# Kernel tuning notes

Hardware: AMD Instinct MI355X
Metric: run time of the kernel (lower is better)

The kernel has to match this reference:

```python
import jax, jax.numpy as jnp
import numpy as np

FEAT = 512   # PLIP backbone dim
HID = 256
N_CLS_HEADS = 11   # each 3 classes -> 33 logits
N_REG_HEADS = 55   # each 1 output

def _xavier(key, shape):
    fan_in, fan_out = shape[0], shape[1]
    limit = float(np.sqrt(6.0 / (fan_in + fan_out)))
    return jax.random.uniform(key, shape, jnp.float32, -limit, limit)

def setup_inputs() -> dict:
    key = jax.random.key(0)
    ks = jax.random.split(key, 8)
    N = 200000
    x = jax.random.normal(ks[0], (1, N, FEAT), jnp.float32)
    return {
        'x': x,
        'W1': _xavier(ks[1], (FEAT, HID)), 'b1': jnp.zeros((HID,), jnp.float32),
        'Wa': _xavier(ks[2], (HID, HID)), 'ba': jnp.zeros((HID,), jnp.float32),
        'Wb': _xavier(ks[3], (HID, HID)), 'bb': jnp.zeros((HID,), jnp.float32),
        'Wc': _xavier(ks[4], (HID, 1)),  'bc': jnp.zeros((1,), jnp.float32),
        'Wr': _xavier(ks[5], (HID, HID)), 'br': jnp.zeros((HID,), jnp.float32),
        # 11 classifier heads (3 classes each) stacked into one [256, 33] GEMM
        'Wcls': _xavier(ks[6], (HID, 3 * N_CLS_HEADS)), 'bcls': jnp.zeros((3 * N_CLS_HEADS,), jnp.float32),
        'Wreg': _xavier(ks[7], (HID, N_REG_HEADS)), 'breg': jnp.zeros((N_REG_HEADS,), jnp.float32),
    }

def reference(x, W1, b1, Wa, ba, Wb, bb, Wc, bc, Wr, br, Wcls, bcls, Wreg, breg):
    xp = x[0]                                   # [N, 512]
    h = jax.nn.relu(xp @ W1 + b1)               # [N, 256]  (dropout inactive at eval)
    a = jnp.tanh(h @ Wa + ba)                   # [N, 256]
    b = jax.nn.sigmoid(h @ Wb + bb)             # [N, 256]
    A_raw = ((a * b) @ Wc + bc).T               # [1, N]
    A = jax.nn.softmax(A_raw, axis=1)           # [1, N]
    global_feat = A @ h                         # [1, 256]
    hr = jax.nn.relu(global_feat @ Wr + br)     # [1, 256]
    cls_logits = hr @ Wcls + bcls               # [1, 33] = 11 heads x 3 classes
    reg_values = (hr @ Wreg + breg)[0]          # [55]   (per-head squeeze(1))
    return A, global_feat, cls_logits, reg_values
```

## Files before the change

kernel.cpp:

```cpp
#include <hip/hip_runtime.h>
#include <stdint.h>

#define FEAT 512
#define HID  256
#define TILE 64
#define G1   768

typedef __attribute__((ext_vector_type(8))) short   short8;
typedef __attribute__((ext_vector_type(4))) float   floatx4;

__device__ inline unsigned short f2bf(float x){
  union { float f; uint32_t u; } v; v.f = x;
  uint32_t u = v.u;
  u += 0x7FFFu + ((u >> 16) & 1u);
  return (unsigned short)(u >> 16);
}
__device__ inline float bf2f(unsigned short h){
  union { uint32_t u; float f; } v; v.u = ((uint32_t)h) << 16;
  return v.f;
}
__device__ inline float sigm_f(float x){ return 1.f/(1.f + __expf(-x)); }
__device__ inline float tanh_f(float x){ return 2.f/(1.f + __expf(-2.f*x)) - 1.f; }

__global__ void prep_weights(const float* __restrict__ W1, const float* __restrict__ Wa,
                             const float* __restrict__ Wb,
                             unsigned short* __restrict__ W1bf,
                             unsigned short* __restrict__ Wabf,
                             unsigned short* __restrict__ Wbbf){
  int t = blockIdx.x*256 + threadIdx.x;
  const float* src; unsigned short* dst; int g;
  if      (t < 16384){ src = W1; dst = W1bf; g = t; }
  else if (t < 24576){ src = Wa; dst = Wabf; g = t - 16384; }
  else if (t < 32768){ src = Wb; dst = Wbbf; g = t - 24576; }
  else return;
  int lane = g & 63, nt = (g >> 6) & 15, kb = g >> 10;
  int col  = nt*16 + (lane & 15);
  int row0 = kb*32 + (lane >> 4)*8;
  unsigned short* d = dst + (size_t)g*8;
  const float*    s = src + (size_t)row0*HID + col;
  #pragma unroll
  for (int j = 0; j < 8; ++j) d[j] = f2bf(s[(size_t)j*HID]);
}

__global__ __launch_bounds__(256, 3) void fused_main(
    const float* __restrict__ x,
    const float* __restrict__ b1, const float* __restrict__ ba,
    const float* __restrict__ bb, const float* __restrict__ Wc,
    const float* __restrict__ bc,
    const unsigned short* __restrict__ W1bf,
    const unsigned short* __restrict__ Wabf,
    const unsigned short* __restrict__ Wbbf,
    float* __restrict__ s_buf, float* __restrict__ partials, int ntiles)
{
  __shared__ alignas(16) unsigned short Hs[64][264];
  __shared__ alignas(16) unsigned short Ws[8192];
  __shared__ float pbuf[4][16];

  const int tid  = threadIdx.x;
  const int wave = tid >> 6, lane = tid & 63;
  const int quad = lane >> 4, l15 = lane & 15;

  float m_run = -INFINITY, l_run = 0.f;
  float g0 = 0.f, g1 = 0.f, g2 = 0.f, g3 = 0.f;
  const float bcv = bc[0];

  for (int t = blockIdx.x; t < ntiles; t += gridDim.x){
    const int tokw = t*TILE + wave*16;

    floatx4 acc[16];
    #pragma unroll
    for (int nt = 0; nt < 16; ++nt){
      float bv = b1[nt*16 + l15];
      floatx4 tmp = {bv, bv, bv, bv};
      acc[nt] = tmp;
    }
    const float* xrow = x + (size_t)(tokw + l15)*FEAT + quad*8;
    #pragma unroll 1
    for (int kb = 0; kb < 16; ++kb){
      __syncthreads();
      { const short8* srcv = (const short8*)(W1bf + (size_t)kb*8192);
        short8* dstv = (short8*)Ws;
        #pragma unroll
        for (int c = 0; c < 4; ++c) dstv[tid + 256*c] = srcv[tid + 256*c]; }
      __syncthreads();
      const float* xp = xrow + kb*32;
      float4 xa = *(const float4*)xp;
      float4 xb = *(const float4*)(xp + 4);
      union { short8 v; unsigned short u[8]; } af;
      af.u[0]=f2bf(xa.x); af.u[1]=f2bf(xa.y); af.u[2]=f2bf(xa.z); af.u[3]=f2bf(xa.w);
      af.u[4]=f2bf(xb.x); af.u[5]=f2bf(xb.y); af.u[6]=f2bf(xb.z); af.u[7]=f2bf(xb.w);
      #pragma unroll
      for (int nt = 0; nt < 16; ++nt){
        short8 bfv = *(const short8*)&Ws[nt*512 + lane*8];
        acc[nt] = __builtin_amdgcn_mfma_f32_16x16x32_bf16(af.v, bfv, acc[nt], 0, 0, 0);
      }
    }
    #pragma unroll
    for (int nt = 0; nt < 16; ++nt){
      #pragma unroll
      for (int r = 0; r < 4; ++r){
        float hv = fmaxf(acc[nt][r], 0.f);
        Hs[wave*16 + quad*4 + r][nt*16 + l15] = f2bf(hv);
      }
    }

    float sp0 = 0.f, sp1 = 0.f, sp2 = 0.f, sp3 = 0.f;
    #pragma unroll 1
    for (int nh = 0; nh < 2; ++nh){
      floatx4 aacc[8], bacc[8];
      #pragma unroll
      for (int nt = 0; nt < 8; ++nt){
        int col = (nh*8 + nt)*16 + l15;
        float av = ba[col], bv = bb[col];
        floatx4 ta = {av, av, av, av}; aacc[nt] = ta;
        floatx4 tb = {bv, bv, bv, bv}; bacc[nt] = tb;
      }
      #pragma unroll 1
      for (int kb = 0; kb < 8; ++kb){
        __syncthreads();
        { const short8* sA = (const short8*)(Wabf + (size_t)(kb*16 + nh*8)*512);
          const short8* sB = (const short8*)(Wbbf + (size_t)(kb*16 + nh*8)*512);
          short8* dstv = (short8*)Ws;
          dstv[tid]       = sA[tid];
          dstv[tid + 256] = sA[tid + 256];
          dstv[tid + 512] = sB[tid];
          dstv[tid + 768] = sB[tid + 256]; }
        __syncthreads();
        short8 af = *(const short8*)&Hs[wave*16 + l15][kb*32 + quad*8];
        #pragma unroll
        for (int nt = 0; nt < 8; ++nt){
          short8 bA = *(const short8*)&Ws[nt*512 + lane*8];
          short8 bB = *(const short8*)&Ws[4096 + nt*512 + lane*8];
          aacc[nt] = __builtin_amdgcn_mfma_f32_16x16x32_bf16(af, bA, aacc[nt], 0, 0, 0);
          bacc[nt] = __builtin_amdgcn_mfma_f32_16x16x32_bf16(af, bB, bacc[nt], 0, 0, 0);
        }
      }
      #pragma unroll
      for (int nt = 0; nt < 8; ++nt){
        int col = (nh*8 + nt)*16 + l15;
        float wcv = Wc[col];
        sp0 += tanh_f(aacc[nt][0]) * sigm_f(bacc[nt][0]) * wcv;
        sp1 += tanh_f(aacc[nt][1]) * sigm_f(bacc[nt][1]) * wcv;
        sp2 += tanh_f(aacc[nt][2]) * sigm_f(bacc[nt][2]) * wcv;
        sp3 += tanh_f(aacc[nt][3]) * sigm_f(bacc[nt][3]) * wcv;
      }
    }
    #pragma unroll
    for (int mk = 1; mk < 16; mk <<= 1){
      sp0 += __shfl_xor(sp0, mk, 64);
      sp1 += __shfl_xor(sp1, mk, 64);
      sp2 += __shfl_xor(sp2, mk, 64);
      sp3 += __shfl_xor(sp3, mk, 64);
    }
    float s0 = sp0 + bcv, s1 = sp1 + bcv, s2 = sp2 + bcv, s3 = sp3 + bcv;
    if (l15 == 0){
      float* sb = s_buf + tokw + quad*4;
      sb[0] = s0; sb[1] = s1; sb[2] = s2; sb[3] = s3;
    }
    float tmax = fmaxf(fmaxf(s0, s1), fmaxf(s2, s3));
    tmax = fmaxf(tmax, __shfl_xor(tmax, 16, 64));
    tmax = fmaxf(tmax, __shfl_xor(tmax, 32, 64));
    float m_new = fmaxf(m_run, tmax);
    float alpha = __expf(m_run - m_new);
    float p0 = __expf(s0 - m_new), p1 = __expf(s1 - m_new);
    float p2 = __expf(s2 - m_new), p3 = __expf(s3 - m_new);
    float psum = p0 + p1 + p2 + p3;
    psum += __shfl_xor(psum, 16, 64);
    psum += __shfl_xor(psum, 32, 64);
    l_run = l_run*alpha + psum;
    m_run = m_new;
    if (l15 == 0){
      pbuf[wave][quad*4+0] = p0; pbuf[wave][quad*4+1] = p1;
      pbuf[wave][quad*4+2] = p2; pbuf[wave][quad*4+3] = p3;
    }
    g0 *= alpha; g1 *= alpha; g2 *= alpha; g3 *= alpha;
    #pragma unroll
    for (int rw = 0; rw < 16; ++rw){
      float pr = pbuf[wave][rw];
      const unsigned short* hp = &Hs[wave*16 + rw][lane*4];
      g0 += pr*bf2f(hp[0]); g1 += pr*bf2f(hp[1]);
      g2 += pr*bf2f(hp[2]); g3 += pr*bf2f(hp[3]);
    }
  }

  __syncthreads();
  float* fred = (float*)Ws;
  if (lane == 0) fred[wave] = m_run;
  __syncthreads();
  float M = fmaxf(fmaxf(fred[0], fred[1]), fmaxf(fred[2], fred[3]));
  float sc = (m_run == -INFINITY) ? 0.f : __expf(m_run - M);
  if (lane == 0) fred[4 + wave] = l_run * sc;
  fred[8 + wave*256 + lane*4 + 0] = g0*sc;
  fred[8 + wave*256 + lane*4 + 1] = g1*sc;
  fred[8 + wave*256 + lane*4 + 2] = g2*sc;
  fred[8 + wave*256 + lane*4 + 3] = g3*sc;
  __syncthreads();
  float gsum = fred[8 + 0*256 + tid] + fred[8 + 1*256 + tid]
             + fred[8 + 2*256 + tid] + fred[8 + 3*256 + tid];
  float* P = partials + (size_t)blockIdx.x*258;
  if (tid == 0){ P[0] = M; P[1] = fred[4] + fred[5] + fred[6] + fred[7]; }
  P[2 + tid] = gsum;
}

__global__ void reduce_heads(const float* __restrict__ partials,
    const float* __restrict__ Wr,   const float* __restrict__ br,
    const float* __restrict__ Wcls, const float* __restrict__ bcls,
    const float* __restrict__ Wreg, const float* __restrict__ breg,
    float* __restrict__ out, float* __restrict__ ML, int ntok)
{
  __shared__ float red[256];
  __shared__ float scw[G1];
  __shared__ float gf[256];
  __shared__ float hr[256];
  int t = threadIdx.x;

  float lm = -INFINITY;
  for (int i = t; i < G1; i += 256) lm = fmaxf(lm, partials[(size_t)i*258]);
  red[t] = lm; __syncthreads();
  for (int s = 128; s > 0; s >>= 1){ if (t < s) red[t] = fmaxf(red[t], red[t+s]); __syncthreads(); }
  float M = red[0];
  __syncthreads();

  float ll = 0.f;
  for (int i = t; i < G1; i += 256){
    float w = __expf(partials[(size_t)i*258] - M);
    scw[i] = w;
    ll += partials[(size_t)i*258 + 1] * w;
  }
  red[t] = ll; __syncthreads();
  for (int s = 128; s > 0; s >>= 1){ if (t < s) red[t] += red[t+s]; __syncthreads(); }
  float L = red[0];

  float g = 0.f;
  for (int i = 0; i < G1; ++i) g += partials[(size_t)i*258 + 2 + t] * scw[i];
  float gfv = g / L;
  gf[t] = gfv;
  out[ntok + t] = gfv;
  if (t == 0){ ML[0] = M; ML[1] = 1.f / L; }
  __syncthreads();

  float h = br[t];
  for (int c = 0; c < 256; ++c) h += gf[c] * Wr[c*256 + t];
  h = fmaxf(h, 0.f);
  hr[t] = h; __syncthreads();

  if (t < 33){
    float v = bcls[t];
    for (int j = 0; j < 256; ++j) v += hr[j] * Wcls[j*33 + t];
    out[ntok + 256 + t] = v;
  }
  if (t < 55){
    float v = breg[t];
    for (int j = 0; j < 256; ++j) v += hr[j] * Wreg[j*55 + t];
    out[ntok + 289 + t] = v;
  }
}

__global__ void finalize_A(const float* __restrict__ s_buf, const float* __restrict__ ML,
                           float* __restrict__ out, int ntok){
  int i = blockIdx.x*256 + threadIdx.x;
  if (i < ntok) out[i] = __expf(s_buf[i] - ML[0]) * ML[1];
}

extern "C" void kernel_launch(void* const* d_in, const int* in_sizes, int n_in,
                              void* d_out, int out_size, void* d_ws, size_t ws_size,
                              hipStream_t stream){
  (void)n_in; (void)out_size; (void)ws_size;
  const float* x    = (const float*)d_in[0];
  const float* W1   = (const float*)d_in[1];
  const float* b1   = (const float*)d_in[2];
  const float* Wa   = (const float*)d_in[3];
  const float* ba   = (const float*)d_in[4];
  const float* Wb   = (const float*)d_in[5];
  const float* bb   = (const float*)d_in[6];
  const float* Wc   = (const float*)d_in[7];
  const float* bc   = (const float*)d_in[8];
  const float* Wr   = (const float*)d_in[9];
  const float* br   = (const float*)d_in[10];
  const float* Wcls = (const float*)d_in[11];
  const float* bcls = (const float*)d_in[12];
  const float* Wreg = (const float*)d_in[13];
  const float* breg = (const float*)d_in[14];
  float* out = (float*)d_out;

  const int ntok   = in_sizes[0] / FEAT;
  const int ntiles = ntok / TILE;

  char* ws = (char*)d_ws;
  float* s_buf = (float*)ws;
  size_t off = (size_t)ntok * 4;
  float* partials = (float*)(ws + off); off += (size_t)G1*258*4;
  float* ML = (float*)(ws + off); off += 16;
  unsigned short* W1bf = (unsigned short*)(ws + off); off += (size_t)FEAT*HID*2;
  unsigned short* Wabf = (unsigned short*)(ws + off); off += (size_t)HID*HID*2;
  unsigned short* Wbbf = (unsigned short*)(ws + off); off += (size_t)HID*HID*2;

  prep_weights<<<128, 256, 0, stream>>>(W1, Wa, Wb, W1bf, Wabf, Wbbf);
  fused_main<<<G1, 256, 0, stream>>>(x, b1, ba, bb, Wc, bc, W1bf, Wabf, Wbbf,
                                     s_buf, partials, ntiles);
  reduce_heads<<<1, 256, 0, stream>>>(partials, Wr, br, Wcls, bcls, Wreg, breg,
                                      out, ML, ntok);
  finalize_A<<<(ntok + 255)/256, 256, 0, stream>>>(s_buf, ML, out, ntok);
}
```

Baseline: 749.8 us.

## Drop LDS weight staging, process 32-token strips per wave with register-prefetched x

The main kernel no longer stages weight blocks into shared memory behind block-wide barriers. Each wave now reads the bf16 weight fragments straight from global/L2 and handles two 16-token strips at once, so each weight fragment feeds two MFMAs. x loads are double-buffered in registers, and a single-strip path handles the tail. The grid shrinks to 512 blocks with launch bounds of 2 per SIMD, and the reduce kernel is widened to 1024 threads with split reductions. This removes barrier stalls and LDS traffic, at the cost of many more global weight loads and higher register pressure, which lowers occupancy.

After: 866.9 us. 15.6% more time.

```diff
diff --git a/kernel.cpp b/kernel.cpp
--- a/kernel.cpp
+++ b/kernel.cpp
@@ -3,8 +3,7 @@
 
 #define FEAT 512
 #define HID  256
-#define TILE 64
-#define G1   768
+#define G1   512
 
 typedef __attribute__((ext_vector_type(8))) short   short8;
 typedef __attribute__((ext_vector_type(4))) float   floatx4;
@@ -21,6 +20,13 @@
 }
 __device__ inline float sigm_f(float x){ return 1.f/(1.f + __expf(-x)); }
 __device__ inline float tanh_f(float x){ return 2.f/(1.f + __expf(-2.f*x)) - 1.f; }
+
+__device__ inline short8 pack_bf8(float4 a, float4 b){
+  union { short8 v; unsigned short u[8]; } r;
+  r.u[0]=f2bf(a.x); r.u[1]=f2bf(a.y); r.u[2]=f2bf(a.z); r.u[3]=f2bf(a.w);
+  r.u[4]=f2bf(b.x); r.u[5]=f2bf(b.y); r.u[6]=f2bf(b.z); r.u[7]=f2bf(b.w);
+  return r.v;
+}
 
 __global__ void prep_weights(const float* __restrict__ W1, const float* __restrict__ Wa,
                              const float* __restrict__ Wb,
@@ -42,7 +48,207 @@
   for (int j = 0; j < 8; ++j) d[j] = f2bf(s[(size_t)j*HID]);
 }
 
-__global__ __launch_bounds__(256, 3) void fused_main(
+template<bool TWO>
+__device__ __forceinline__ void do_tile(
+    const float* __restrict__ x, int tok0,
+    const unsigned short* __restrict__ W1bf,
+    const unsigned short* __restrict__ Wabf,
+    const unsigned short* __restrict__ Wbbf,
+    const float* __restrict__ b1, const float* __restrict__ ba,
+    const float* __restrict__ bb, const float* __restrict__ Wc, float bcv,
+    float* __restrict__ s_buf,
+    unsigned short (*__restrict__ hs)[264], float* __restrict__ pbufw,
+    int lane, int quad, int l15,
+    float& m_run, float& l_run, float& g0, float& g1, float& g2, float& g3)
+{
+  const short8* w1v = (const short8*)W1bf;
+  const short8* wav = (const short8*)Wabf;
+  const short8* wbv = (const short8*)Wbbf;
+
+  floatx4 acc0[16], acc1[16];
+  #pragma unroll
+  for (int nt = 0; nt < 16; ++nt){
+    float bv = b1[nt*16 + l15];
+    floatx4 t = {bv, bv, bv, bv};
+    acc0[nt] = t;
+    if (TWO) acc1[nt] = t;
+  }
+  const float* xr0 = x + (size_t)(tok0 + l15)*FEAT + quad*8;
+  const float* xr1 = x + (size_t)(tok0 + 16 + l15)*FEAT + quad*8;
+
+  float4 xA0[2], xB0[2], xA1[2], xB1[2];
+  xA0[0] = *(const float4*)(xr0);       xA0[1] = *(const float4*)(xr0 + 4);
+  xB0[0] = *(const float4*)(xr0 + 32);  xB0[1] = *(const float4*)(xr0 + 36);
+  if (TWO){
+    xA1[0] = *(const float4*)(xr1);       xA1[1] = *(const float4*)(xr1 + 4);
+    xB1[0] = *(const float4*)(xr1 + 32);  xB1[1] = *(const float4*)(xr1 + 36);
+  }
+  #pragma unroll 1
+  for (int i = 0; i < 8; ++i){
+    const int kbe = 2*i, kbo = 2*i + 1;
+    short8 af0 = pack_bf8(xA0[0], xA0[1]);
+    short8 af1;
+    if (TWO) af1 = pack_bf8(xA1[0], xA1[1]);
+    if (i < 7){
+      xA0[0] = *(const float4*)(xr0 + (kbe+2)*32);
+      xA0[1] = *(const float4*)(xr0 + (kbe+2)*32 + 4);
+      if (TWO){
+        xA1[0] = *(const float4*)(xr1 + (kbe+2)*32);
+        xA1[1] = *(const float4*)(xr1 + (kbe+2)*32 + 4);
+      }
+    }
+    {
+      const short8* wp = w1v + (size_t)kbe*1024 + lane;
+      #pragma unroll
+      for (int nt = 0; nt < 16; ++nt){
+        short8 wf = wp[nt*64];
+        acc0[nt] = __builtin_amdgcn_mfma_f32_16x16x32_bf16(af0, wf, acc0[nt], 0, 0, 0);
+        if (TWO)
+          acc1[nt] = __builtin_amdgcn_mfma_f32_16x16x32_bf16(af1, wf, acc1[nt], 0, 0, 0);
+      }
+    }
+    short8 bf0 = pack_bf8(xB0[0], xB0[1]);
+    short8 bf1;
+    if (TWO) bf1 = pack_bf8(xB1[0], xB1[1]);
+    if (i < 7){
+      xB0[0] = *(const float4*)(xr0 + (kbo+2)*32);
+      xB0[1] = *(const float4*)(xr0 + (kbo+2)*32 + 4);
+      if (TWO){
+        xB1[0] = *(const float4*)(xr1 + (kbo+2)*32);
+        xB1[1] = *(const float4*)(xr1 + (kbo+2)*32 + 4);
+      }
+    }
+    {
+      const short8* wp = w1v + (size_t)kbo*1024 + lane;
+      #pragma unroll
+      for (int nt = 0; nt < 16; ++nt){
+        short8 wf = wp[nt*64];
+        acc0[nt] = __builtin_amdgcn_mfma_f32_16x16x32_bf16(bf0, wf, acc0[nt], 0, 0, 0);
+        if (TWO)
+          acc1[nt] = __builtin_amdgcn_mfma_f32_16x16x32_bf16(bf1, wf, acc1[nt], 0, 0, 0);
+      }
+    }
+  }
+  #pragma unroll
+  for (int nt = 0; nt < 16; ++nt){
+    #pragma unroll
+    for (int r = 0; r < 4; ++r){
+      hs[quad*4 + r][nt*16 + l15] = f2bf(fmaxf(acc0[nt][r], 0.f));
+      if (TWO) hs[16 + quad*4 + r][nt*16 + l15] = f2bf(fmaxf(acc1[nt][r], 0.f));
+    }
+  }
+
+  float s00=0.f,s01=0.f,s02=0.f,s03=0.f, s10=0.f,s11=0.f,s12=0.f,s13=0.f;
+  #pragma unroll 1
+  for (int nh = 0; nh < 2; ++nh){
+    floatx4 aa0[8], ab0[8], aa1[8], ab1[8];
+    #pragma unroll
+    for (int nt = 0; nt < 8; ++nt){
+      int col = (nh*8 + nt)*16 + l15;
+      float av = ba[col], bv = bb[col];
+      floatx4 ta = {av, av, av, av};
+      floatx4 tb = {bv, bv, bv, bv};
+      aa0[nt] = ta; ab0[nt] = tb;
+      if (TWO){ aa1[nt] = ta; ab1[nt] = tb; }
+    }
+    short8 hf0 = *(const short8*)&hs[l15][quad*8];
+    short8 hf1;
+    if (TWO) hf1 = *(const short8*)&hs[16 + l15][quad*8];
+    #pragma unroll 1
+    for (int kb = 0; kb < 8; ++kb){
+      short8 cf0 = hf0, cf1;
+      if (TWO) cf1 = hf1;
+      if (kb < 7){
+        hf0 = *(const short8*)&hs[l15][(kb+1)*32 + quad*8];
+        if (TWO) hf1 = *(const short8*)&hs[16 + l15][(kb+1)*32 + quad*8];
+      }
+      const short8* wpa = wav + (size_t)(kb*16 + nh*8)*64 + lane;
+      const short8* wpb = wbv + (size_t)(kb*16 + nh*8)*64 + lane;
+      #pragma unroll
+      for (int nt = 0; nt < 8; ++nt){
+        short8 wfa = wpa[nt*64];
+        short8 wfb = wpb[nt*64];
+        aa0[nt] = __builtin_amdgcn_mfma_f32_16x16x32_bf16(cf0, wfa, aa0[nt], 0, 0, 0);
+        ab0[nt] = __builtin_amdgcn_mfma_f32_16x16x32_bf16(cf0, wfb, ab0[nt], 0, 0, 0);
+        if (TWO){
+          aa1[nt] = __builtin_amdgcn_mfma_f32_16x16x32_bf16(cf1, wfa, aa1[nt], 0, 0, 0);
+          ab1[nt] = __builtin_amdgcn_mfma_f32_16x16x32_bf16(cf1, wfb, ab1[nt], 0, 0, 0);
+        }
+      }
+    }
+    #pragma unroll
+    for (int nt = 0; nt < 8; ++nt){
+      float wcv = Wc[(nh*8 + nt)*16 + l15];
+      s00 += tanh_f(aa0[nt][0]) * sigm_f(ab0[nt][0]) * wcv;
+      s01 += tanh_f(aa0[nt][1]) * sigm_f(ab0[nt][1]) * wcv;
+      s02 += tanh_f(aa0[nt][2]) * sigm_f(ab0[nt][2]) * wcv;
+      s03 += tanh_f(aa0[nt][3]) * sigm_f(ab0[nt][3]) * wcv;
+      if (TWO){
+        s10 += tanh_f(aa1[nt][0]) * sigm_f(ab1[nt][0]) * wcv;
+        s11 += tanh_f(aa1[nt][1]) * sigm_f(ab1[nt][1]) * wcv;
+        s12 += tanh_f(aa1[nt][2]) * sigm_f(ab1[nt][2]) * wcv;
+        s13 += tanh_f(aa1[nt][3]) * sigm_f(ab1[nt][3]) * wcv;
+      }
+    }
+  }
+  #pragma unroll
+  for (int mk = 1; mk < 16; mk <<= 1){
+    s00 += __shfl_xor(s00, mk, 64); s01 += __shfl_xor(s01, mk, 64);
+    s02 += __shfl_xor(s02, mk, 64); s03 += __shfl_xor(s03, mk, 64);
+    if (TWO){
+      s10 += __shfl_xor(s10, mk, 64); s11 += __shfl_xor(s11, mk, 64);
+      s12 += __shfl_xor(s12, mk, 64); s13 += __shfl_xor(s13, mk, 64);
+    }
+  }
+  s00 += bcv; s01 += bcv; s02 += bcv; s03 += bcv;
+  if (TWO){ s10 += bcv; s11 += bcv; s12 += bcv; s13 += bcv; }
+  if (l15 == 0){
+    float* sb = s_buf + tok0 + quad*4;
+    sb[0] = s00; sb[1] = s01; sb[2] = s02; sb[3] = s03;
+    if (TWO){
+      float* sb1 = s_buf + tok0 + 16 + quad*4;
+      sb1[0] = s10; sb1[1] = s11; sb1[2] = s12; sb1[3] = s13;
+    }
+  }
+  float tmax = fmaxf(fmaxf(s00, s01), fmaxf(s02, s03));
+  if (TWO) tmax = fmaxf(tmax, fmaxf(fmaxf(s10, s11), fmaxf(s12, s13)));
+  tmax = fmaxf(tmax, __shfl_xor(tmax, 16, 64));
+  tmax = fmaxf(tmax, __shfl_xor(tmax, 32, 64));
+  float m_new = fmaxf(m_run, tmax);
+  float alpha = __expf(m_run - m_new);
+  float p00 = __expf(s00 - m_new), p01 = __expf(s01 - m_new);
+  float p02 = __expf(s02 - m_new), p03 = __expf(s03 - m_new);
+  float psum = p00 + p01 + p02 + p03;
+  float p10, p11, p12, p13;
+  if (TWO){
+    p10 = __expf(s10 - m_new); p11 = __expf(s11 - m_new);
+    p12 = __expf(s12 - m_new); p13 = __expf(s13 - m_new);
+    psum += p10 + p11 + p12 + p13;
+  }
+  psum += __shfl_xor(psum, 16, 64);
+  psum += __shfl_xor(psum, 32, 64);
+  l_run = l_run*alpha + psum;
+  m_run = m_new;
+  if (l15 == 0){
+    pbufw[quad*4+0] = p00; pbufw[quad*4+1] = p01;
+    pbufw[quad*4+2] = p02; pbufw[quad*4+3] = p03;
+    if (TWO){
+      pbufw[16+quad*4+0] = p10; pbufw[16+quad*4+1] = p11;
+      pbufw[16+quad*4+2] = p12; pbufw[16+quad*4+3] = p13;
+    }
+  }
+  g0 *= alpha; g1 *= alpha; g2 *= alpha; g3 *= alpha;
+  constexpr int NR = TWO ? 32 : 16;
+  #pragma unroll
+  for (int rw = 0; rw < NR; ++rw){
+    float pr = pbufw[rw];
+    const unsigned short* hp = &hs[rw][lane*4];
+    g0 += pr*bf2f(hp[0]); g1 += pr*bf2f(hp[1]);
+    g2 += pr*bf2f(hp[2]); g3 += pr*bf2f(hp[3]);
+  }
+}
+
+__global__ __launch_bounds__(256, 2) void fused_main(
     const float* __restrict__ x,
     const float* __restrict__ b1, const float* __restrict__ ba,
     const float* __restrict__ bb, const float* __restrict__ Wc,
@@ -50,141 +256,41 @@
     const unsigned short* __restrict__ W1bf,
     const unsigned short* __restrict__ Wabf,
     const unsigned short* __restrict__ Wbbf,
-    float* __restrict__ s_buf, float* __restrict__ partials, int ntiles)
+    float* __restrict__ s_buf, float* __restrict__ partials, int ntok)
 {
-  __shared__ alignas(16) unsigned short Hs[64][264];
-  __shared__ alignas(16) unsigned short Ws[8192];
-  __shared__ float pbuf[4][16];
+  __shared__ alignas(16) unsigned short Hs[4][32][264];
+  __shared__ float pbuf[4][32];
 
   const int tid  = threadIdx.x;
   const int wave = tid >> 6, lane = tid & 63;
   const int quad = lane >> 4, l15 = lane & 15;
+  const int wid  = blockIdx.x*4 + wave;
+  const int nw   = gridDim.x << 2;
 
   float m_run = -INFINITY, l_run = 0.f;
   float g0 = 0.f, g1 = 0.f, g2 = 0.f, g3 = 0.f;
   const float bcv = bc[0];
 
-  for (int t = blockIdx.x; t < ntiles; t += gridDim.x){
-    const int tokw = t*TILE + wave*16;
-
-    floatx4 acc[16];
-    #pragma unroll
-    for (int nt = 0; nt < 16; ++nt){
-      float bv = b1[nt*16 + l15];
-      floatx4 tmp = {bv, bv, bv, bv};
-      acc[nt] = tmp;
-    }
-    const float* xrow = x + (size_t)(tokw + l15)*FEAT + quad*8;
-    #pragma unroll 1
-    for (int kb = 0; kb < 16; ++kb){
-      __syncthreads();
-      { const short8* srcv = (const short8*)(W1bf + (size_t)kb*8192);
-        short8* dstv = (short8*)Ws;
-        #pragma unroll
-        for (int c = 0; c < 4; ++c) dstv[tid + 256*c] = srcv[tid + 256*c]; }
-      __syncthreads();
-      const float* xp = xrow + kb*32;
-      float4 xa = *(const float4*)xp;
-      float4 xb = *(const float4*)(xp + 4);
-      union { short8 v; unsigned short u[8]; } af;
-      af.u[0]=f2bf(xa.x); af.u[1]=f2bf(xa.y); af.u[2]=f2bf(xa.z); af.u[3]=f2bf(xa.w);
-      af.u[4]=f2bf(xb.x); af.u[5]=f2bf(xb.y); af.u[6]=f2bf(xb.z); af.u[7]=f2bf(xb.w);
-      #pragma unroll
-      for (int nt = 0; nt < 16; ++nt){
-        short8 bfv = *(const short8*)&Ws[nt*512 + lane*8];
-        acc[nt] = __builtin_amdgcn_mfma_f32_16x16x32_bf16(af.v, bfv, acc[nt], 0, 0, 0);
-      }
-    }
-    #pragma unroll
-    for (int nt = 0; nt < 16; ++nt){
-      #pragma unroll
-      for (int r = 0; r < 4; ++r){
-        float hv = fmaxf(acc[nt][r], 0.f);
-        Hs[wave*16 + quad*4 + r][nt*16 + l15] = f2bf(hv);
-      }
-    }
-
-    float sp0 = 0.f, sp1 = 0.f, sp2 = 0.f, sp3 = 0.f;
-    #pragma unroll 1
-    for (int nh = 0; nh < 2; ++nh){
-      floatx4 aacc[8], bacc[8];
-      #pragma unroll
-      for (int nt = 0; nt < 8; ++nt){
-        int col = (nh*8 + nt)*16 + l15;
-        float av = ba[col], bv = bb[col];
-        floatx4 ta = {av, av, av, av}; aacc[nt] = ta;
-        floatx4 tb = {bv, bv, bv, bv}; bacc[nt] = tb;
-      }
-      #pragma unroll 1
-      for (int kb = 0; kb < 8; ++kb){
-        __syncthreads();
-        { const short8* sA = (const short8*)(Wabf + (size_t)(kb*16 + nh*8)*512);
-          const short8* sB = (const short8*)(Wbbf + (size_t)(kb*16 + nh*8)*512);
-          short8* dstv = (short8*)Ws;
-          dstv[tid]       = sA[tid];
-          dstv[tid + 256] = sA[tid + 256];
-          dstv[tid + 512] = sB[tid];
-          dstv[tid + 768] = sB[tid + 256]; }
-        __syncthreads();
-        short8 af = *(const short8*)&Hs[wave*16 + l15][kb*32 + quad*8];
-        #pragma unroll
-        for (int nt = 0; nt < 8; ++nt){
-          short8 bA = *(const short8*)&Ws[nt*512 + lane*8];
-          short8 bB = *(const short8*)&Ws[4096 + nt*512 + lane*8];
-          aacc[nt] = __builtin_amdgcn_mfma_f32_16x16x32_bf16(af, bA, aacc[nt], 0, 0, 0);
-          bacc[nt] = __builtin_amdgcn_mfma_f32_16x16x32_bf16(af, bB, bacc[nt], 0, 0, 0);
-        }
-      }
-      #pragma unroll
-      for (int nt = 0; nt < 8; ++nt){
-        int col = (nh*8 + nt)*16 + l15;
-        float wcv = Wc[col];
-        sp0 += tanh_f(aacc[nt][0]) * sigm_f(bacc[nt][0]) * wcv;
-        sp1 += tanh_f(aacc[nt][1]) * sigm_f(bacc[nt][1]) * wcv;
-        sp2 += tanh_f(aacc[nt][2]) * sigm_f(bacc[nt][2]) * wcv;
-        sp3 += tanh_f(aacc[nt][3]) * sigm_f(bacc[nt][3]) * wcv;
-      }
-    }
-    #pragma unroll
-    for (int mk = 1; mk < 16; mk <<= 1){
-      sp0 += __shfl_xor(sp0, mk, 64);
-      sp1 += __shfl_xor(sp1, mk, 64);
-      sp2 += __shfl_xor(sp2, mk, 64);
-      sp3 += __shfl_xor(sp3, mk, 64);
-    }
-    float s0 = sp0 + bcv, s1 = sp1 + bcv, s2 = sp2 + bcv, s3 = sp3 + bcv;
-    if (l15 == 0){
-      float* sb = s_buf + tokw + quad*4;
-      sb[0] = s0; sb[1] = s1; sb[2] = s2; sb[3] = s3;
-    }
-    float tmax = fmaxf(fmaxf(s0, s1), fmaxf(s2, s3));
-    tmax = fmaxf(tmax, __shfl_xor(tmax, 16, 64));
-    tmax = fmaxf(tmax, __shfl_xor(tmax, 32, 64));
-    float m_new = fmaxf(m_run, tmax);
-    float alpha = __expf(m_run - m_new);
-    float p0 = __expf(s0 - m_new), p1 = __expf(s1 - m_new);
-    float p2 = __expf(s2 - m_new), p3 = __expf(s3 - m_new);
-    float psum = p0 + p1 + p2 + p3;
-    psum += __shfl_xor(psum, 16, 64);
-    psum += __shfl_xor(psum, 32, 64);
-    l_run = l_run*alpha + psum;
-    m_run = m_new;
-    if (l15 == 0){
-      pbuf[wave][quad*4+0] = p0; pbuf[wave][quad*4+1] = p1;
-      pbuf[wave][quad*4+2] = p2; pbuf[wave][quad*4+3] = p3;
-    }
-    g0 *= alpha; g1 *= alpha; g2 *= alpha; g3 *= alpha;
-    #pragma unroll
-    for (int rw = 0; rw < 16; ++rw){
-      float pr = pbuf[wave][rw];
-      const unsigned short* hp = &Hs[wave*16 + rw][lane*4];
-      g0 += pr*bf2f(hp[0]); g1 += pr*bf2f(hp[1]);
-      g2 += pr*bf2f(hp[2]); g3 += pr*bf2f(hp[3]);
-    }
-  }
-
-  __syncthreads();
-  float* fred = (float*)Ws;
+  const int nstrips  = ntok >> 4;
+  const int rounds   = (nstrips >> 1) / nw;
+  const int tailbase = rounds * nw * 2;
+  const int ntail    = nstrips - tailbase;
+
+  for (int r = 0; r < rounds; ++r){
+    int tok0 = (r*nw + wid) * 32;
+    do_tile<true>(x, tok0, W1bf, Wabf, Wbbf, b1, ba, bb, Wc, bcv,
+                  s_buf, Hs[wave], pbuf[wave], lane, quad, l15,
+                  m_run, l_run, g0, g1, g2, g3);
+  }
+  if (wid < ntail){
+    int tok0 = (tailbase + wid) * 16;
+    do_tile<false>(x, tok0, W1bf, Wabf, Wbbf, b1, ba, bb, Wc, bcv,
+                   s_buf, Hs[wave], pbuf[wave], lane, quad, l15,
+                   m_run, l_run, g0, g1, g2, g3);
+  }
+
+  __syncthreads();
+  float* fred = reinterpret_cast<float*>(&Hs[0][0][0]);
   if (lane == 0) fred[wave] = m_run;
   __syncthreads();
   float M = fmaxf(fmaxf(fred[0], fred[1]), fmaxf(fred[2], fred[3]));
@@ -202,57 +308,73 @@
   P[2 + tid] = gsum;
 }
 
-__global__ void reduce_heads(const float* __restrict__ partials,
+__global__ __launch_bounds__(1024) void reduce_heads(const float* __restrict__ partials,
     const float* __restrict__ Wr,   const float* __restrict__ br,
     const float* __restrict__ Wcls, const float* __restrict__ bcls,
     const float* __restrict__ Wreg, const float* __restrict__ breg,
     float* __restrict__ out, float* __restrict__ ML, int ntok)
 {
-  __shared__ float red[256];
+  __shared__ float red[1024];
   __shared__ float scw[G1];
   __shared__ float gf[256];
   __shared__ float hr[256];
-  int t = threadIdx.x;
+  const int t = threadIdx.x;
 
   float lm = -INFINITY;
-  for (int i = t; i < G1; i += 256) lm = fmaxf(lm, partials[(size_t)i*258]);
+  for (int i = t; i < G1; i += 1024) lm = fmaxf(lm, partials[(size_t)i*258]);
   red[t] = lm; __syncthreads();
-  for (int s = 128; s > 0; s >>= 1){ if (t < s) red[t] = fmaxf(red[t], red[t+s]); __syncthreads(); }
+  for (int s = 512; s > 0; s >>= 1){ if (t < s) red[t] = fmaxf(red[t], red[t+s]); __syncthreads(); }
   float M = red[0];
   __syncthreads();
 
   float ll = 0.f;
-  for (int i = t; i < G1; i += 256){
+  for (int i = t; i < G1; i += 1024){
     float w = __expf(partials[(size_t)i*258] - M);
     scw[i] = w;
     ll += partials[(size_t)i*258 + 1] * w;
   }
   red[t] = ll; __syncthreads();
-  for (int s = 128; s > 0; s >>= 1){ if (t < s) red[t] += red[t+s]; __syncthreads(); }
+  for (int s = 512; s > 0; s >>= 1){ if (t < s) red[t] += red[t+s]; __syncthreads(); }
   float L = red[0];
-
+  __syncthreads();
+
+  const int col = t & 255, grp = t >> 8;
   float g = 0.f;
-  for (int i = 0; i < G1; ++i) g += partials[(size_t)i*258 + 2 + t] * scw[i];
-  float gfv = g / L;
-  gf[t] = gfv;
-  out[ntok + t] = gfv;
-  if (t == 0){ ML[0] = M; ML[1] = 1.f / L; }
-  __syncthreads();
-
-  float h = br[t];
-  for (int c = 0; c < 256; ++c) h += gf[c] * Wr[c*256 + t];
-  h = fmaxf(h, 0.f);
-  hr[t] = h; __syncthreads();
-
-  if (t < 33){
-    float v = bcls[t];
-    for (int j = 0; j < 256; ++j) v += hr[j] * Wcls[j*33 + t];
-    out[ntok + 256 + t] = v;
-  }
-  if (t < 55){
-    float v = breg[t];
-    for (int j = 0; j < 256; ++j) v += hr[j] * Wreg[j*55 + t];
-    out[ntok + 289 + t] = v;
+  #pragma unroll 4
+  for (int i = grp; i < G1; i += 4) g += partials[(size_t)i*258 + 2 + col] * scw[i];
+  red[t] = g; __syncthreads();
+  if (grp == 0){
+    float gfv = (red[col] + red[256+col] + red[512+col] + red[768+col]) / L;
+    gf[col] = gfv;
+    out[ntok + col] = gfv;
+    if (col == 0){ ML[0] = M; ML[1] = 1.f / L; }
+  }
+  __syncthreads();
+
+  float h = 0.f;
+  #pragma unroll 8
+  for (int c = grp*64; c < grp*64 + 64; ++c) h += gf[c] * Wr[(size_t)c*256 + col];
+  red[t] = h; __syncthreads();
+  if (grp == 0){
+    float hv = red[col] + red[256+col] + red[512+col] + red[768+col] + br[col];
+    hr[col] = fmaxf(hv, 0.f);
+  }
+  __syncthreads();
+
+  const int o = t >> 3, sl = t & 7;
+  if (o < 33){
+    float v = 0.f;
+    #pragma unroll 8
+    for (int j = sl; j < 256; j += 8) v += hr[j] * Wcls[(size_t)j*33 + o];
+    v += __shfl_xor(v, 1, 64); v += __shfl_xor(v, 2, 64); v += __shfl_xor(v, 4, 64);
+    if (sl == 0) out[ntok + 256 + o] = v + bcls[o];
+  } else if (o >= 64 && o < 64 + 55){
+    int oo = o - 64;
+    float v = 0.f;
+    #pragma unroll 8
+    for (int j = sl; j < 256; j += 8) v += hr[j] * Wreg[(size_t)j*55 + oo];
+    v += __shfl_xor(v, 1, 64); v += __shfl_xor(v, 2, 64); v += __shfl_xor(v, 4, 64);
+    if (sl == 0) out[ntok + 289 + oo] = v + breg[oo];
   }
 }
 
@@ -283,8 +405,7 @@
   const float* breg = (const float*)d_in[14];
   float* out = (float*)d_out;
 
-  const int ntok   = in_sizes[0] / FEAT;
-  const int ntiles = ntok / TILE;
+  const int ntok = in_sizes[0] / FEAT;
 
   char* ws = (char*)d_ws;
   float* s_buf = (float*)ws;
@@ -297,8 +418,8 @@
 
   prep_weights<<<128, 256, 0, stream>>>(W1, Wa, Wb, W1bf, Wabf, Wbbf);
   fused_main<<<G1, 256, 0, stream>>>(x, b1, ba, bb, Wc, bc, W1bf, Wabf, Wbbf,
-                                     s_buf, partials, ntiles);
-  reduce_heads<<<1, 256, 0, stream>>>(partials, Wr, br, Wcls, bcls, Wreg, breg,
-                                      out, ML, ntok);
+                                     s_buf, partials, ntok);
+  reduce_heads<<<1, 1024, 0, stream>>>(partials, Wr, br, Wcls, bcls, Wreg, breg,
+                                       out, ML, ntok);
   finalize_A<<<(ntok + 255)/256, 256, 0, stream>>>(s_buf, ML, out, ntok);
 }
```

## Double-buffer weight tiles via direct global-to-LDS loads and prefetch x up front

Applied to the files above, without the earlier changes.

Weight tiles for the three GEMMs are now staged through a double-buffered LDS area using global_load_lds, with the next tile's load issued before the current tile's MFMAs. The old register round-trip and the paired __syncthreads per k-step are replaced by explicit waitcnt plus s_barrier. The x row fragment for all 16 k-blocks is loaded and converted to bf16 up front, which hides its latency but raises register pressure, so occupancy is lowered to 2 blocks and the grid to 512 blocks. The single-block reduction kernel is widened to 1024 threads so the partial sums and head GEMVs are split across more threads.

Result: slower. 965.2 us (+28.7%).

```diff
diff --git a/kernel.cpp b/kernel.cpp
--- a/kernel.cpp
+++ b/kernel.cpp
@@ -4,10 +4,11 @@
 #define FEAT 512
 #define HID  256
 #define TILE 64
-#define G1   768
+#define G1   512
 
 typedef __attribute__((ext_vector_type(8))) short   short8;
 typedef __attribute__((ext_vector_type(4))) float   floatx4;
+typedef unsigned int u32;
 
 __device__ inline unsigned short f2bf(float x){
   union { float f; uint32_t u; } v; v.f = x;
@@ -21,6 +22,21 @@
 }
 __device__ inline float sigm_f(float x){ return 1.f/(1.f + __expf(-x)); }
 __device__ inline float tanh_f(float x){ return 2.f/(1.f + __expf(-2.f*x)) - 1.f; }
+
+__device__ inline short8 pack_bf8(float4 a, float4 b){
+  union { short8 v; unsigned short u[8]; } r;
+  r.u[0]=f2bf(a.x); r.u[1]=f2bf(a.y); r.u[2]=f2bf(a.z); r.u[3]=f2bf(a.w);
+  r.u[4]=f2bf(b.x); r.u[5]=f2bf(b.y); r.u[6]=f2bf(b.z); r.u[7]=f2bf(b.w);
+  return r.v;
+}
+
+__device__ __forceinline__ void gl_lds16(const void* g, void* l){
+  __builtin_amdgcn_global_load_lds(
+      (const __attribute__((address_space(1))) u32*)g,
+      (__attribute__((address_space(3))) u32*)l, 16, 0, 0);
+}
+
+#define SCHED_FENCE() __builtin_amdgcn_sched_barrier(0)
 
 __global__ void prep_weights(const float* __restrict__ W1, const float* __restrict__ Wa,
                              const float* __restrict__ Wb,
@@ -42,7 +58,7 @@
   for (int j = 0; j < 8; ++j) d[j] = f2bf(s[(size_t)j*HID]);
 }
 
-__global__ __launch_bounds__(256, 3) void fused_main(
+__global__ __launch_bounds__(256, 2) void fused_main(
     const float* __restrict__ x,
     const float* __restrict__ b1, const float* __restrict__ ba,
     const float* __restrict__ bb, const float* __restrict__ Wc,
@@ -53,7 +69,7 @@
     float* __restrict__ s_buf, float* __restrict__ partials, int ntiles)
 {
   __shared__ alignas(16) unsigned short Hs[64][264];
-  __shared__ alignas(16) unsigned short Ws[8192];
+  __shared__ alignas(16) unsigned short Ws[2][8192];
   __shared__ float pbuf[4][16];
 
   const int tid  = threadIdx.x;
@@ -66,6 +82,17 @@
 
   for (int t = blockIdx.x; t < ntiles; t += gridDim.x){
     const int tokw = t*TILE + wave*16;
+
+    short8 xf[16];
+    {
+      const float* xr = x + (size_t)(tokw + l15)*FEAT + quad*8;
+      #pragma unroll
+      for (int kb = 0; kb < 16; ++kb){
+        float4 a = *(const float4*)(xr + kb*32);
+        float4 b = *(const float4*)(xr + kb*32 + 4);
+        xf[kb] = pack_bf8(a, b);
+      }
+    }
 
     floatx4 acc[16];
     #pragma unroll
@@ -74,34 +101,48 @@
       floatx4 tmp = {bv, bv, bv, bv};
       acc[nt] = tmp;
     }
-    const float* xrow = x + (size_t)(tokw + l15)*FEAT + quad*8;
-    #pragma unroll 1
+    #pragma unroll
+    for (int c = 0; c < 4; ++c)
+      gl_lds16(W1bf + (wave*4 + c)*512 + lane*8, &Ws[0][(wave*4 + c)*512]);
+
+    #pragma unroll
     for (int kb = 0; kb < 16; ++kb){
-      __syncthreads();
-      { const short8* srcv = (const short8*)(W1bf + (size_t)kb*8192);
-        short8* dstv = (short8*)Ws;
+      if (kb < 15){
+        const unsigned short* src = W1bf + (size_t)(kb+1)*8192;
+        unsigned short* dst = Ws[(kb+1) & 1];
         #pragma unroll
-        for (int c = 0; c < 4; ++c) dstv[tid + 256*c] = srcv[tid + 256*c]; }
-      __syncthreads();
-      const float* xp = xrow + kb*32;
-      float4 xa = *(const float4*)xp;
-      float4 xb = *(const float4*)(xp + 4);
-      union { short8 v; unsigned short u[8]; } af;
-      af.u[0]=f2bf(xa.x); af.u[1]=f2bf(xa.y); af.u[2]=f2bf(xa.z); af.u[3]=f2bf(xa.w);
-      af.u[4]=f2bf(xb.x); af.u[5]=f2bf(xb.y); af.u[6]=f2bf(xb.z); af.u[7]=f2bf(xb.w);
+        for (int c = 0; c < 4; ++c)
+          gl_lds16(src + (wave*4 + c)*512 + lane*8, dst + (wave*4 + c)*512);
+        SCHED_FENCE();
+        asm volatile("s_waitcnt vmcnt(4)" ::: "memory");
+      } else {
+        SCHED_FENCE();
+        asm volatile("s_waitcnt vmcnt(0)" ::: "memory");
+      }
+      __builtin_amdgcn_s_barrier();
+      SCHED_FENCE();
+      const unsigned short* wsb = Ws[kb & 1];
       #pragma unroll
       for (int nt = 0; nt < 16; ++nt){
-        short8 bfv = *(const short8*)&Ws[nt*512 + lane*8];
-        acc[nt] = __builtin_amdgcn_mfma_f32_16x16x32_bf16(af.v, bfv, acc[nt], 0, 0, 0);
-      }
+        short8 wf = *(const short8*)(wsb + nt*512 + lane*8);
+        acc[nt] = __builtin_amdgcn_mfma_f32_16x16x32_bf16(xf[kb], wf, acc[nt], 0, 0, 0);
+      }
+      SCHED_FENCE();
+      __builtin_amdgcn_s_barrier();
+    }
+
+    #pragma unroll
+    for (int c = 0; c < 4; ++c){
+      int chunk = wave*4 + c;
+      const unsigned short* s8 = (chunk < 8) ? (Wabf + chunk*512)
+                                             : (Wbbf + (chunk-8)*512);
+      gl_lds16(s8 + lane*8, &Ws[0][chunk*512]);
     }
     #pragma unroll
     for (int nt = 0; nt < 16; ++nt){
       #pragma unroll
-      for (int r = 0; r < 4; ++r){
-        float hv = fmaxf(acc[nt][r], 0.f);
-        Hs[wave*16 + quad*4 + r][nt*16 + l15] = f2bf(hv);
-      }
+      for (int r = 0; r < 4; ++r)
+        Hs[wave*16 + quad*4 + r][nt*16 + l15] = f2bf(fmaxf(acc[nt][r], 0.f));
     }
 
     float sp0 = 0.f, sp1 = 0.f, sp2 = 0.f, sp3 = 0.f;
@@ -117,28 +158,42 @@
       }
       #pragma unroll 1
       for (int kb = 0; kb < 8; ++kb){
-        __syncthreads();
-        { const short8* sA = (const short8*)(Wabf + (size_t)(kb*16 + nh*8)*512);
-          const short8* sB = (const short8*)(Wbbf + (size_t)(kb*16 + nh*8)*512);
-          short8* dstv = (short8*)Ws;
-          dstv[tid]       = sA[tid];
-          dstv[tid + 256] = sA[tid + 256];
-          dstv[tid + 512] = sB[tid];
-          dstv[tid + 768] = sB[tid + 256]; }
-        __syncthreads();
-        short8 af = *(const short8*)&Hs[wave*16 + l15][kb*32 + quad*8];
+        int s = nh*8 + kb;
+        if (s < 15){
+          int s2 = s + 1, nh2 = s2 >> 3, kb2 = s2 & 7;
+          const unsigned short* srcA = Wabf + (size_t)(kb2*16 + nh2*8)*512;
+          const unsigned short* srcB = Wbbf + (size_t)(kb2*16 + nh2*8)*512;
+          unsigned short* dst = Ws[s2 & 1];
+          #pragma unroll
+          for (int c = 0; c < 4; ++c){
+            int chunk = wave*4 + c;
+            const unsigned short* s8 = (chunk < 8) ? (srcA + chunk*512)
+                                                   : (srcB + (chunk-8)*512);
+            gl_lds16(s8 + lane*8, dst + chunk*512);
+          }
+          SCHED_FENCE();
+          asm volatile("s_waitcnt vmcnt(4)" ::: "memory");
+        } else {
+          SCHED_FENCE();
+          asm volatile("s_waitcnt vmcnt(0)" ::: "memory");
+        }
+        __builtin_amdgcn_s_barrier();
+        SCHED_FENCE();
+        const unsigned short* wsb = Ws[s & 1];
+        short8 hf = *(const short8*)&Hs[wave*16 + l15][kb*32 + quad*8];
         #pragma unroll
         for (int nt = 0; nt < 8; ++nt){
-          short8 bA = *(const short8*)&Ws[nt*512 + lane*8];
-          short8 bB = *(const short8*)&Ws[4096 + nt*512 + lane*8];
-          aacc[nt] = __builtin_amdgcn_mfma_f32_16x16x32_bf16(af, bA, aacc[nt], 0, 0, 0);
-          bacc[nt] = __builtin_amdgcn_mfma_f32_16x16x32_bf16(af, bB, bacc[nt], 0, 0, 0);
+          short8 wfa = *(const short8*)(wsb + nt*512 + lane*8);
+          short8 wfb = *(const short8*)(wsb + 4096 + nt*512 + lane*8);
+          aacc[nt] = __builtin_amdgcn_mfma_f32_16x16x32_bf16(hf, wfa, aacc[nt], 0, 0, 0);
+          bacc[nt] = __builtin_amdgcn_mfma_f32_16x16x32_bf16(hf, wfb, bacc[nt], 0, 0, 0);
         }
+        SCHED_FENCE();
+        __builtin_amdgcn_s_barrier();
       }
       #pragma unroll
       for (int nt = 0; nt < 8; ++nt){
-        int col = (nh*8 + nt)*16 + l15;
-        float wcv = Wc[col];
+        float wcv = Wc[(nh*8 + nt)*16 + l15];
         sp0 += tanh_f(aacc[nt][0]) * sigm_f(bacc[nt][0]) * wcv;
         sp1 += tanh_f(aacc[nt][1]) * sigm_f(bacc[nt][1]) * wcv;
         sp2 += tanh_f(aacc[nt][2]) * sigm_f(bacc[nt][2]) * wcv;
@@ -202,57 +257,73 @@
   P[2 + tid] = gsum;
 }
 
-__global__ void reduce_heads(const float* __restrict__ partials,
+__global__ __launch_bounds__(1024) void reduce_heads(const float* __restrict__ partials,
     const float* __restrict__ Wr,   const float* __restrict__ br,
     const float* __restrict__ Wcls, const float* __restrict__ bcls,
     const float* __restrict__ Wreg, const float* __restrict__ breg,
     float* __restrict__ out, float* __restrict__ ML, int ntok)
 {
-  __shared__ float red[256];
+  __shared__ float red[1024];
   __shared__ float scw[G1];
   __shared__ float gf[256];
   __shared__ float hr[256];
-  int t = threadIdx.x;
+  const int t = threadIdx.x;
 
   float lm = -INFINITY;
-  for (int i = t; i < G1; i += 256) lm = fmaxf(lm, partials[(size_t)i*258]);
+  for (int i = t; i < G1; i += 1024) lm = fmaxf(lm, partials[(size_t)i*258]);
   red[t] = lm; __syncthreads();
-  for (int s = 128; s > 0; s >>= 1){ if (t < s) red[t] = fmaxf(red[t], red[t+s]); __syncthreads(); }
+  for (int s = 512; s > 0; s >>= 1){ if (t < s) red[t] = fmaxf(red[t], red[t+s]); __syncthreads(); }
   float M = red[0];
   __syncthreads();
 
   float ll = 0.f;
-  for (int i = t; i < G1; i += 256){
+  for (int i = t; i < G1; i += 1024){
     float w = __expf(partials[(size_t)i*258] - M);
     scw[i] = w;
     ll += partials[(size_t)i*258 + 1] * w;
   }
   red[t] = ll; __syncthreads();
-  for (int s = 128; s > 0; s >>= 1){ if (t < s) red[t] += red[t+s]; __syncthreads(); }
+  for (int s = 512; s > 0; s >>= 1){ if (t < s) red[t] += red[t+s]; __syncthreads(); }
   float L = red[0];
-
+  __syncthreads();
+
+  const int col = t & 255, grp = t >> 8;
   float g = 0.f;
-  for (int i = 0; i < G1; ++i) g += partials[(size_t)i*258 + 2 + t] * scw[i];
-  float gfv = g / L;
-  gf[t] = gfv;
-  out[ntok + t] = gfv;
-  if (t == 0){ ML[0] = M; ML[1] = 1.f / L; }
-  __syncthreads();
-
-  float h = br[t];
-  for (int c = 0; c < 256; ++c) h += gf[c] * Wr[c*256 + t];
-  h = fmaxf(h, 0.f);
-  hr[t] = h; __syncthreads();
-
-  if (t < 33){
-    float v = bcls[t];
-    for (int j = 0; j < 256; ++j) v += hr[j] * Wcls[j*33 + t];
-    out[ntok + 256 + t] = v;
-  }
-  if (t < 55){
-    float v = breg[t];
-    for (int j = 0; j < 256; ++j) v += hr[j] * Wreg[j*55 + t];
-    out[ntok + 289 + t] = v;
+  #pragma unroll 4
+  for (int i = grp; i < G1; i += 4) g += partials[(size_t)i*258 + 2 + col] * scw[i];
+  red[t] = g; __syncthreads();
+  if (grp == 0){
+    float gfv = (red[col] + red[256+col] + red[512+col] + red[768+col]) / L;
+    gf[col] = gfv;
+    out[ntok + col] = gfv;
+    if (col == 0){ ML[0] = M; ML[1] = 1.f / L; }
+  }
+  __syncthreads();
+
+  float h = 0.f;
+  #pragma unroll 8
+  for (int c = grp*64; c < grp*64 + 64; ++c) h += gf[c] * Wr[(size_t)c*256 + col];
+  red[t] = h; __syncthreads();
+  if (grp == 0){
+    float hv = red[col] + red[256+col] + red[512+col] + red[768+col] + br[col];
+    hr[col] = fmaxf(hv, 0.f);
+  }
+  __syncthreads();
+
+  const int o = t >> 3, sl = t & 7;
+  if (o < 33){
+    float v = 0.f;
+    #pragma unroll 8
+    for (int j = sl; j < 256; j += 8) v += hr[j] * Wcls[(size_t)j*33 + o];
+    v += __shfl_xor(v, 1, 64); v += __shfl_xor(v, 2, 64); v += __shfl_xor(v, 4, 64);
+    if (sl == 0) out[ntok + 256 + o] = v + bcls[o];
+  } else if (o >= 64 && o < 64 + 55){
+    int oo = o - 64;
+    float v = 0.f;
+    #pragma unroll 8
+    for (int j = sl; j < 256; j += 8) v += hr[j] * Wreg[(size_t)j*55 + oo];
+    v += __shfl_xor(v, 1, 64); v += __shfl_xor(v, 2, 64); v += __shfl_xor(v, 4, 64);
+    if (sl == 0) out[ntok + 289 + oo] = v + breg[oo];
   }
 }
 
@@ -298,7 +369,7 @@
   prep_weights<<<128, 256, 0, stream>>>(W1, Wa, Wb, W1bf, Wabf, Wbbf);
   fused_main<<<G1, 256, 0, stream>>>(x, b1, ba, bb, Wc, bc, W1bf, Wabf, Wbbf,
                                      s_buf, partials, ntiles);
-  reduce_heads<<<1, 256, 0, stream>>>(partials, Wr, br, Wcls, bcls, Wreg, breg,
-                                      out, ML, ntok);
+  reduce_heads<<<1, 1024, 0, stream>>>(partials, Wr, br, Wcls, bcls, Wreg, breg,
+                                       out, ML, ntok);
   finalize_A<<<(ntok + 255)/256, 256, 0, stream>>>(s_buf, ML, out, ntok);
 }
```
